# Kernel tuning notes

Hardware: AMD Instinct MI355X
Metric: run time of the kernel (lower is better)

Reference implementation:

```python
import jax, jax.numpy as jnp
import numpy as np
from jax import lax

B, T, D, LD, K = 128, 1024, 256, 512, 128
RD = LD + K  # 640 residual-LSTM width
PAD = 15     # (31 - 1) // 2 'same' padding for the LSA location conv


def _gru(x, h, wih, whh, bih, bhh):
    # torch.nn.GRUCell semantics, gate order [r, z, n]
    gi = x @ wih.T + bih
    gh = h @ whh.T + bhh
    ir, iz, inn = jnp.split(gi, 3, axis=-1)
    hr, hz, hn = jnp.split(gh, 3, axis=-1)
    r = jax.nn.sigmoid(ir + hr)
    z = jax.nn.sigmoid(iz + hz)
    n = jnp.tanh(inn + r * hn)
    return (1.0 - z) * n + z * h


def _lstm(x, h, c, wih, whh, bih, bhh):
    # torch.nn.LSTMCell semantics, gate order [i, f, g, o]
    g = x @ wih.T + bih + h @ whh.T + bhh
    i, f, gg, o = jnp.split(g, 4, axis=-1)
    c2 = jax.nn.sigmoid(f) * c + jax.nn.sigmoid(i) * jnp.tanh(gg)
    h2 = jax.nn.sigmoid(o) * jnp.tanh(c2)
    return h2, c2


def _forward(encoder_seq, encoder_seq_proj, prenet_in, attn_hidden, rnn1_h, rnn1_c,
             rnn2_h, rnn2_c, res_h, res_c, context_vec, cumulative, attn_prev,
             fc1_w, fc1_b, fc2_w, fc2_b, gru_wih, gru_whh, gru_bih, gru_bhh,
             conv_w, L_w, L_b, W_w, W_b, v_w, ri_w, ri_b,
             r1_wih, r1_whh, r1_bih, r1_bhh, r2_wih, r2_whh, r2_bih, r2_bhh,
             res_wih, res_whh, res_bih, res_bhh, stop_w, stop_b):
    # PreNet (dropout p = 0 in Decoder.__init__, so pure tanh-MLP)
    p = jnp.tanh(prenet_in @ fc1_w.T + fc1_b)
    prenet_out = jnp.tanh(p @ fc2_w.T + fc2_b)                     # [B, D//2]
    # Attention GRU
    attn_in = jnp.concatenate([context_vec, prenet_out], axis=-1)  # [B, D + D//2]
    attn_h = _gru(attn_in, attn_hidden, gru_wih, gru_whh, gru_bih, gru_bhh)  # [B, D]
    # LSA location-sensitive attention (cumulative/attn_prev are zeros at t=0)
    pq = (attn_h @ W_w.T + W_b)[:, None, :]                        # [B, 1, D]
    loc = jnp.stack([cumulative, attn_prev], axis=1)               # [B, 2, T]
    conv_out = lax.conv_general_dilated(loc, conv_w, (1,), [(PAD, PAD)],
                                        dimension_numbers=('NCH', 'OIH', 'NCH'))  # [B, 32, T]
    ploc = jnp.swapaxes(conv_out, 1, 2) @ L_w.T + L_b              # [B, T, D]
    u = jnp.squeeze(jnp.tanh(pq + encoder_seq_proj + ploc) @ v_w.T, -1)  # [B, T]
    sig = jax.nn.sigmoid(u)
    scores = sig / jnp.sum(sig, axis=1, keepdims=True)             # [B, T]
    cum_new = cumulative + scores
    context = jnp.einsum('bt,btd->bd', scores, encoder_seq)        # [B, D]
    # rnn_input projection + two residual LSTM cells (eval: no zoneout)
    x = jnp.concatenate([context, attn_h], axis=1) @ ri_w.T + ri_b  # [B, LD]
    h1, c1 = _lstm(x, rnn1_h, rnn1_c, r1_wih, r1_whh, r1_bih, r1_bhh)
    x = x + h1
    h2, c2 = _lstm(x, rnn2_h, rnn2_c, r2_wih, r2_whh, r2_bih, r2_bhh)
    x = x + h2
    # 4-layer residual LSTM stack on [prenet_in, x]
    res_x = jnp.concatenate([prenet_in, x], axis=1)                # [B, RD]
    hs, cs = [], []
    for i in range(4):
        hi, ci = _lstm(res_x, res_h[i], res_c[i], res_wih[i], res_whh[i], res_bih[i], res_bhh[i])
        res_x = res_x + hi
        hs.append(hi)
        cs.append(ci)
    cond = res_x                                                   # cond_features [B, RD]
    stop = jax.nn.sigmoid(cond @ stop_w.T + stop_b)                # [B, 1]
    return (cond, stop, scores, attn_h, h1, c1, h2, c2,
            jnp.stack(hs), jnp.stack(cs), context, cum_new)


def setup_inputs() -> dict:
    keys = iter(jax.random.split(jax.random.key(0), 64))
    nxt = lambda: next(keys)
    rn = lambda s: jax.random.normal(nxt(), s, jnp.float32)
    wp = lambda s: rn(s) * 0.02
    return {
        'encoder_seq': rn((B, T, D)),
        'encoder_seq_proj': rn((B, T, D)),
        'prenet_in': rn((B, K)),
        'attn_hidden': rn((B, D)),
        'rnn1_h': rn((B, LD)), 'rnn1_c': rn((B, LD)),
        'rnn2_h': rn((B, LD)), 'rnn2_c': rn((B, LD)),
        'res_h': rn((4, B, RD)), 'res_c': rn((4, B, RD)),
        'context_vec': rn((B, D)),
        'cumulative': jnp.zeros((B, T), jnp.float32),
        'attn_prev': jnp.zeros((B, T), jnp.float32),
        'fc1_w': wp((256, K)), 'fc1_b': jnp.zeros((256,), jnp.float32),
        'fc2_w': wp((D // 2, 256)), 'fc2_b': jnp.zeros((D // 2,), jnp.float32),
        'gru_wih': wp((3 * D, D + D // 2)), 'gru_whh': wp((3 * D, D)),
        'gru_bih': jnp.zeros((3 * D,), jnp.float32), 'gru_bhh': jnp.zeros((3 * D,), jnp.float32),
        'conv_w': wp((32, 2, 31)),
        'L_w': wp((D, 32)), 'L_b': jnp.zeros((D,), jnp.float32),
        'W_w': wp((D, D)), 'W_b': jnp.zeros((D,), jnp.float32),
        'v_w': wp((1, D)),
        'ri_w': wp((LD, 2 * D)), 'ri_b': jnp.zeros((LD,), jnp.float32),
        'r1_wih': wp((4 * LD, LD)), 'r1_whh': wp((4 * LD, LD)),
        'r1_bih': jnp.zeros((4 * LD,), jnp.float32), 'r1_bhh': jnp.zeros((4 * LD,), jnp.float32),
        'r2_wih': wp((4 * LD, LD)), 'r2_whh': wp((4 * LD, LD)),
        'r2_bih': jnp.zeros((4 * LD,), jnp.float32), 'r2_bhh': jnp.zeros((4 * LD,), jnp.float32),
        'res_wih': wp((4, 4 * RD, RD)), 'res_whh': wp((4, 4 * RD, RD)),
        'res_bih': jnp.zeros((4, 4 * RD), jnp.float32), 'res_bhh': jnp.zeros((4, 4 * RD), jnp.float32),
        'stop_w': wp((1, RD)), 'stop_b': jnp.zeros((1,), jnp.float32),
    }


def reference(encoder_seq, encoder_seq_proj, prenet_in, attn_hidden, rnn1_h, rnn1_c,
              rnn2_h, rnn2_c, res_h, res_c, context_vec, cumulative, attn_prev,
              fc1_w, fc1_b, fc2_w, fc2_b, gru_wih, gru_whh, gru_bih, gru_bhh,
              conv_w, L_w, L_b, W_w, W_b, v_w, ri_w, ri_b,
              r1_wih, r1_whh, r1_bih, r1_bhh, r2_wih, r2_whh, r2_bih, r2_bhh,
              res_wih, res_whh, res_bih, res_bhh, stop_w, stop_b):
    return _forward(encoder_seq, encoder_seq_proj, prenet_in, attn_hidden, rnn1_h, rnn1_c,
                    rnn2_h, rnn2_c, res_h, res_c, context_vec, cumulative, attn_prev,
                    fc1_w, fc1_b, fc2_w, fc2_b, gru_wih, gru_whh, gru_bih, gru_bhh,
                    conv_w, L_w, L_b, W_w, W_b, v_w, ri_w, ri_b,
                    r1_wih, r1_whh, r1_bih, r1_bhh, r2_wih, r2_whh, r2_bih, r2_bhh,
                    res_wih, res_whh, res_bih, res_bhh, stop_w, stop_b)
```

## Files before the change

kernel.cpp:

```cpp
#include <hip/hip_runtime.h>

#define DEV __device__ __forceinline__

typedef __attribute__((ext_vector_type(8))) short short8;
typedef __attribute__((ext_vector_type(4))) float f32x4;

DEV float fast_rcp(float x) { return __builtin_amdgcn_rcpf(x); }
DEV float sigm(float x) { return fast_rcp(1.0f + __expf(-x)); }
DEV float tanhf_fast(float x) { return 1.0f - 2.0f * fast_rcp(1.0f + __expf(2.0f * x)); }

DEV short f2bf(float f) {
    unsigned u = __float_as_uint(f);
    unsigned r = (u + 0x7FFFu + ((u >> 16) & 1u)) >> 16;
    return (short)r;
}
DEV float bf2f(short h) {
    return __uint_as_float(((unsigned)(unsigned short)h) << 16);
}
DEV void split1(float f, short& h, short& l) {
    h = f2bf(f);
    l = f2bf(f - bf2f(h));
}
DEV void split8(const float4& x0, const float4& x1, short8& h, short8& l) {
    float fv[8] = {x0.x, x0.y, x0.z, x0.w, x1.x, x1.y, x1.z, x1.w};
#pragma unroll
    for (int j = 0; j < 8; ++j) { short hh, ll; split1(fv[j], hh, ll); h[j] = hh; l[j] = ll; }
}
#define MFMA16 __builtin_amdgcn_mfma_f32_16x16x32_bf16
DEV f32x4 mfma3(const short8& ah, const short8& al, const short8& bh, const short8& bl, f32x4 acc) {
    acc = MFMA16(ah, bh, acc, 0, 0, 0);
    acc = MFMA16(al, bh, acc, 0, 0, 0);
    acc = MFMA16(ah, bl, acc, 0, 0, 0);
    return acc;
}

DEV void gemm_core(int bx,
                   const float* __restrict__ A1, int K1,
                   const float* __restrict__ W1, int ldw1,
                   const float* __restrict__ A2, int K2,
                   const float* __restrict__ W2, int ldw2,
                   float* __restrict__ Cp, int N, int KS, int KC)
{
    const int tid = threadIdx.x;
    const int chunk = bx % KS;
    const int n0 = (bx / KS) * 32;
    const int kbeg = chunk * KC;
    const int w = tid >> 6, lane = tid & 63;
    const int q = lane >> 4, r = lane & 15;
    const int m_base = w * 32;

    f32x4 acc[2][2];
#pragma unroll
    for (int mt = 0; mt < 2; ++mt)
#pragma unroll
        for (int nt = 0; nt < 2; ++nt)
            acc[mt][nt] = (f32x4){0.f, 0.f, 0.f, 0.f};

    auto load_frag = [&](int kg, float4 (&a)[2][2], float4 (&wv)[2][2]) {
        const float* A; const float* W; int lda, ldw, kc;
        if (kg < K1) { A = A1; W = W1; lda = K1; ldw = ldw1; kc = kg; }
        else         { A = A2; W = W2; lda = K2; ldw = ldw2; kc = kg - K1; }
#pragma unroll
        for (int mt = 0; mt < 2; ++mt) {
            const float* ap = A + (size_t)(m_base + mt * 16 + r) * lda + kc + q * 8;
            a[mt][0] = *(const float4*)ap;
            a[mt][1] = *(const float4*)(ap + 4);
        }
#pragma unroll
        for (int nt = 0; nt < 2; ++nt) {
            const float* wp = W + (size_t)(n0 + nt * 16 + r) * ldw + kc + q * 8;
            wv[nt][0] = *(const float4*)wp;
            wv[nt][1] = *(const float4*)(wp + 4);
        }
    };

    auto compute = [&](const float4 (&a)[2][2], const float4 (&wv)[2][2]) {
        short8 bh[2], bl[2];
#pragma unroll
        for (int nt = 0; nt < 2; ++nt) split8(wv[nt][0], wv[nt][1], bh[nt], bl[nt]);
#pragma unroll
        for (int mt = 0; mt < 2; ++mt) {
            short8 ah, al;
            split8(a[mt][0], a[mt][1], ah, al);
#pragma unroll
            for (int nt = 0; nt < 2; ++nt)
                acc[mt][nt] = mfma3(ah, al, bh[nt], bl[nt], acc[mt][nt]);
        }
    };

    float4 aA[2][2], aB[2][2], wA[2][2], wB[2][2];
    const int nsteps = KC >> 5;

    load_frag(kbeg, aA, wA);
    for (int s = 0; s + 1 < nsteps; ++s) {
        if (s & 1) { load_frag(kbeg + (s + 1) * 32, aA, wA); compute(aB, wB); }
        else       { load_frag(kbeg + (s + 1) * 32, aB, wB); compute(aA, wA); }
    }
    if ((nsteps - 1) & 1) compute(aB, wB);
    else                  compute(aA, wA);

    float* Co = Cp + (size_t)chunk * 128 * N;
#pragma unroll
    for (int mt = 0; mt < 2; ++mt)
#pragma unroll
        for (int nt = 0; nt < 2; ++nt)
#pragma unroll
            for (int i = 0; i < 4; ++i)
                Co[(size_t)(m_base + mt * 16 + q * 4 + i) * N + n0 + nt * 16 + r] = acc[mt][nt][i];
}

__global__ __launch_bounds__(256) void gemm_one_kernel(
    const float* __restrict__ A1, int K1, const float* __restrict__ W1, int ldw1,
    const float* __restrict__ A2, int K2, const float* __restrict__ W2, int ldw2,
    float* __restrict__ Cp, int N, int KS, int KC)
{
    gemm_core(blockIdx.x, A1, K1, W1, ldw1, A2, K2, W2, ldw2, Cp, N, KS, KC);
}

__global__ __launch_bounds__(256) void gemm_gru_kernel(
    const float* __restrict__ ctx, const float* __restrict__ pout,
    const float* __restrict__ h_old,
    const float* __restrict__ wih, const float* __restrict__ whh,
    float* __restrict__ Pa, float* __restrict__ Pb)
{
    if (blockIdx.x < 288)
        gemm_core(blockIdx.x, ctx, 256, wih, 384, pout, 128, wih + 256, 384,
                  Pa, 768, 12, 32);
    else
        gemm_core(blockIdx.x - 288, h_old, 256, whh, 256, nullptr, 0, nullptr, 0,
                  Pb, 768, 8, 32);
}

__global__ void reduce_act_kernel(const float* __restrict__ p, int KS, int MN,
                                  const float* __restrict__ b,
                                  float* __restrict__ out, int N, int act)
{
    int idx = blockIdx.x * 256 + threadIdx.x;
    if (idx >= MN) return;
    int n = idx % N;
    float v = b ? b[n] : 0.f;
    for (int s = 0; s < KS; ++s) v += p[(size_t)s * MN + idx];
    if (act) v = tanhf_fast(v);
    out[idx] = v;
}

__global__ void gru_gate_kernel(const float* __restrict__ gi_p, int KSi,
                                const float* __restrict__ gh_p, int KSh,
                                const float* __restrict__ bih, const float* __restrict__ bhh,
                                const float* __restrict__ h, float* __restrict__ out)
{
    const size_t MN = 128 * 768;
    int m = blockIdx.x, d = threadIdx.x;
    size_t base = (size_t)m * 768 + d;
    float ir = bih[d], iz = bih[256 + d], in = bih[512 + d];
    for (int s = 0; s < KSi; ++s) {
        const float* p = gi_p + s * MN + base;
        ir += p[0]; iz += p[256]; in += p[512];
    }
    float hr = bhh[d], hz = bhh[256 + d], hn = bhh[512 + d];
    for (int s = 0; s < KSh; ++s) {
        const float* p = gh_p + s * MN + base;
        hr += p[0]; hz += p[256]; hn += p[512];
    }
    float r = sigm(ir + hr);
    float z = sigm(iz + hz);
    float n = tanhf_fast(in + r * hn);
    out[m * 256 + d] = (1.f - z) * n + z * h[m * 256 + d];
}

__global__ void lstm_gate_kernel(const float* __restrict__ gp, int KS,
                                 const float* __restrict__ bih, const float* __restrict__ bhh,
                                 const float* __restrict__ c_in,
                                 float* __restrict__ h_out, float* __restrict__ c_out,
                                 const float* __restrict__ xa, int sa,
                                 const float* __restrict__ xb, int sb, int split,
                                 float* __restrict__ x_new, int H)
{
    int d = blockIdx.x * 256 + threadIdx.x;
    int m = blockIdx.y;
    if (d >= H) return;
    const size_t MN = (size_t)128 * 4 * H;
    size_t base = (size_t)m * 4 * H + d;
    float iv = bih[d] + bhh[d];
    float fv = bih[H + d] + bhh[H + d];
    float gv = bih[2 * H + d] + bhh[2 * H + d];
    float ov = bih[3 * H + d] + bhh[3 * H + d];
    for (int s = 0; s < KS; ++s) {
        const float* p = gp + s * MN + base;
        iv += p[0]; fv += p[H]; gv += p[2 * H]; ov += p[3 * H];
    }
    float c2 = sigm(fv) * c_in[(size_t)m * H + d] + sigm(iv) * tanhf_fast(gv);
    float h2 = sigm(ov) * tanhf_fast(c2);
    h_out[(size_t)m * H + d] = h2;
    c_out[(size_t)m * H + d] = c2;
    float xo = (d < split) ? xa[(size_t)m * sa + d] : xb[(size_t)m * sb + d - split];
    x_new[(size_t)m * H + d] = xo + h2;
}

__global__ __launch_bounds__(256) void attn_u_kernel(
    const float* __restrict__ esp, const float* __restrict__ pq,
    const float* __restrict__ Lw, const float* __restrict__ Lb,
    const float* __restrict__ vw, const float* __restrict__ cw,
    const float* __restrict__ cum, const float* __restrict__ prev,
    float* __restrict__ sig_out)
{
    const int b = blockIdx.x >> 4;
    const int t0 = (blockIdx.x & 15) << 6;
    const int tid = threadIdx.x;

    __shared__ float cum_s[94], prev_s[94];
    __shared__ float cw_s[2][32][33];
    __shared__ short conv_bf[64 * 32];
    __shared__ short lw_bf[256 * 32];
    __shared__ float pq_s[256], vw_s[256];

    if (tid < 94) {
        int ti = t0 - 15 + tid;
        cum_s[tid] = (ti >= 0 && ti < 1024) ? cum[b * 1024 + ti] : 0.f;
    } else if (tid >= 128 && tid < 222) {
        int i = tid - 128;
        int ti = t0 - 15 + i;
        prev_s[i] = (ti >= 0 && ti < 1024) ? prev[b * 1024 + ti] : 0.f;
    }
    for (int i = tid; i < 2048; i += 256) {
        int which = i >> 10, c = (i >> 5) & 31, k = i & 31;
        cw_s[which][c][k] = (k < 31) ? cw[(c * 2 + which) * 31 + k] : 0.f;
    }
    {
        const float4* src = (const float4*)Lw;
#pragma unroll
        for (int k = 0; k < 8; ++k) {
            float4 v = src[tid + k * 256];
            int base = (tid + k * 256) * 4;
            lw_bf[base + 0] = f2bf(v.x);
            lw_bf[base + 1] = f2bf(v.y);
            lw_bf[base + 2] = f2bf(v.z);
            lw_bf[base + 3] = f2bf(v.w);
        }
    }
    pq_s[tid] = pq[b * 256 + tid] + Lb[tid];
    vw_s[tid] = vw[tid];
    __syncthreads();

    {
        int c = tid & 31, t8 = (tid >> 5) << 3;
        float a[8] = {0.f, 0.f, 0.f, 0.f, 0.f, 0.f, 0.f, 0.f};
        for (int k = 0; k < 31; ++k) {
            float w0 = cw_s[0][c][k], w1 = cw_s[1][c][k];
#pragma unroll
            for (int j = 0; j < 8; ++j)
                a[j] += w0 * cum_s[t8 + j + k] + w1 * prev_s[t8 + j + k];
        }
#pragma unroll
        for (int j = 0; j < 8; ++j) conv_bf[(t8 + j) * 32 + c] = f2bf(a[j]);
    }
    __syncthreads();

    const int lane = tid & 63, w = tid >> 6;
    const int q = lane >> 4, c16 = lane & 15;
    const int myt = t0 + w * 16 + c16;

    short8 bfrag = *(const short8*)&conv_bf[(w * 16 + c16) * 32 + q * 8];
    const float* er = esp + ((size_t)(b * 1024 + myt) << 8);

    float s = 0.f;
#pragma unroll
    for (int dt = 0; dt < 16; ++dt) {
        short8 afrag = *(const short8*)&lw_bf[(dt * 16 + c16) * 32 + q * 8];
        f32x4 acc = {0.f, 0.f, 0.f, 0.f};
        acc = MFMA16(afrag, bfrag, acc, 0, 0, 0);
        const int d0 = dt * 16 + q * 4;
        float4 e   = *(const float4*)(er + d0);
        float4 pqv = *(const float4*)&pq_s[d0];
        float4 vwv = *(const float4*)&vw_s[d0];
        s += tanhf_fast(pqv.x + e.x + acc[0]) * vwv.x;
        s += tanhf_fast(pqv.y + e.y + acc[1]) * vwv.y;
        s += tanhf_fast(pqv.z + e.z + acc[2]) * vwv.z;
        s += tanhf_fast(pqv.w + e.w + acc[3]) * vwv.w;
    }
    s += __shfl_xor(s, 16);
    s += __shfl_xor(s, 32);
    if (lane < 16)
        sig_out[b * 1024 + t0 + w * 16 + lane] = sigm(s);
}

__global__ void attn_norm_kernel(const float* __restrict__ sig, const float* __restrict__ cum,
                                 float* __restrict__ scores, float* __restrict__ cum_new,
                                 float* __restrict__ ctx)
{
    __shared__ float red[4];
    int b = blockIdx.x, tid = threadIdx.x;
    float4 sv = *(const float4*)&sig[b * 1024 + tid * 4];
    float s = sv.x + sv.y + sv.z + sv.w;
#pragma unroll
    for (int off = 1; off < 64; off <<= 1) s += __shfl_xor(s, off);
    if ((tid & 63) == 0) red[tid >> 6] = s;
    __syncthreads();
    float inv = fast_rcp(red[0] + red[1] + red[2] + red[3]);
    float4 cv = *(const float4*)&cum[b * 1024 + tid * 4];
    float4 sc = {sv.x * inv, sv.y * inv, sv.z * inv, sv.w * inv};
    *(float4*)&scores[b * 1024 + tid * 4] = sc;
    float4 cn = {cv.x + sc.x, cv.y + sc.y, cv.z + sc.z, cv.w + sc.w};
    *(float4*)&cum_new[b * 1024 + tid * 4] = cn;
    ctx[b * 256 + tid] = 0.f;
}

__global__ void attn_ctx_kernel(const float* __restrict__ scores, const float* __restrict__ es,
                                float* __restrict__ ctx)
{
    __shared__ float sc_s[128];
    int b = blockIdx.x >> 3;
    int tbase = (blockIdx.x & 7) * 128;
    int tid = threadIdx.x;
    if (tid < 128) sc_s[tid] = scores[b * 1024 + tbase + tid];
    __syncthreads();
    float a = 0.f;
    const float* ep = es + ((size_t)(b * 1024 + tbase)) * 256 + tid;
#pragma unroll 4
    for (int tt = 0; tt < 128; ++tt)
        a += sc_s[tt] * ep[(size_t)tt * 256];
    atomicAdd(&ctx[b * 256 + tid], a);
}

__global__ void stop_kernel(const float* __restrict__ res, const float* __restrict__ sw,
                            const float* __restrict__ sb, float* __restrict__ stop)
{
    int m = blockIdx.x, lane = threadIdx.x;
    float s = 0.f;
    for (int k = lane; k < 640; k += 64) s += res[m * 640 + k] * sw[k];
#pragma unroll
    for (int off = 1; off < 64; off <<= 1) s += __shfl_xor(s, off);
    if (lane == 0) stop[m] = sigm(s + sb[0]);
}

extern "C" void kernel_launch(void* const* d_in, const int* in_sizes, int n_in,
                              void* d_out, int out_size, void* d_ws, size_t ws_size,
                              hipStream_t stream)
{
    const float* encoder_seq      = (const float*)d_in[0];
    const float* encoder_seq_proj = (const float*)d_in[1];
    const float* prenet_in        = (const float*)d_in[2];
    const float* attn_hidden      = (const float*)d_in[3];
    const float* rnn1_h  = (const float*)d_in[4];
    const float* rnn1_c  = (const float*)d_in[5];
    const float* rnn2_h  = (const float*)d_in[6];
    const float* rnn2_c  = (const float*)d_in[7];
    const float* res_h   = (const float*)d_in[8];
    const float* res_c   = (const float*)d_in[9];
    const float* context_vec = (const float*)d_in[10];
    const float* cumulative  = (const float*)d_in[11];
    const float* attn_prev   = (const float*)d_in[12];
    const float* fc1_w = (const float*)d_in[13];
    const float* fc1_b = (const float*)d_in[14];
    const float* fc2_w = (const float*)d_in[15];
    const float* fc2_b = (const float*)d_in[16];
    const float* gru_wih = (const float*)d_in[17];
    const float* gru_whh = (const float*)d_in[18];
    const float* gru_bih = (const float*)d_in[19];
    const float* gru_bhh = (const float*)d_in[20];
    const float* conv_w = (const float*)d_in[21];
    const float* L_w = (const float*)d_in[22];
    const float* L_b = (const float*)d_in[23];
    const float* W_w = (const float*)d_in[24];
    const float* W_b = (const float*)d_in[25];
    const float* v_w = (const float*)d_in[26];
    const float* ri_w = (const float*)d_in[27];
    const float* ri_b = (const float*)d_in[28];
    const float* r1_wih = (const float*)d_in[29];
    const float* r1_whh = (const float*)d_in[30];
    const float* r1_bih = (const float*)d_in[31];
    const float* r1_bhh = (const float*)d_in[32];
    const float* r2_wih = (const float*)d_in[33];
    const float* r2_whh = (const float*)d_in[34];
    const float* r2_bih = (const float*)d_in[35];
    const float* r2_bhh = (const float*)d_in[36];
    const float* res_wih = (const float*)d_in[37];
    const float* res_whh = (const float*)d_in[38];
    const float* res_bih = (const float*)d_in[39];
    const float* res_bhh = (const float*)d_in[40];
    const float* stop_w = (const float*)d_in[41];
    const float* stop_b = (const float*)d_in[42];

    float* ws  = (float*)d_ws;
    float* out = (float*)d_out;

    const size_t OFF_P     = 0;
    const size_t OFF_POUT  = 32768;
    const size_t OFF_PQ    = 49152;
    const size_t OFF_SIG   = 81920;
    const size_t OFF_X     = 212992;
    const size_t OFF_XB    = 278528;
    const size_t OFF_XC    = 344064;
    const size_t OFF_R0    = 409600;
    const size_t OFF_R1    = 491520;
    const size_t OFF_PART  = 573440;
    const size_t OFF_PARTB = OFF_PART + (size_t)12 * 128 * 768;
    const size_t OFF_PARTH = OFF_PART + (size_t)4 * 128 * 2560;

    const size_t O_COND   = 0;
    const size_t O_STOP   = 81920;
    const size_t O_SCORES = 82048;
    const size_t O_ATTNH  = 213120;
    const size_t O_H1     = 245888;
    const size_t O_C1     = 311424;
    const size_t O_H2     = 376960;
    const size_t O_C2     = 442496;
    const size_t O_HS     = 508032;
    const size_t O_CS     = 835712;
    const size_t O_CTX    = 1163392;
    const size_t O_CUM    = 1196160;

    gemm_one_kernel<<<8 * 4, 256, 0, stream>>>(
        prenet_in, 128, fc1_w, 128, nullptr, 0, nullptr, 0,
        ws + OFF_PART, 256, 4, 32);
    reduce_act_kernel<<<128, 256, 0, stream>>>(ws + OFF_PART, 4, 128 * 256, fc1_b,
                                               ws + OFF_P, 256, 1);
    gemm_one_kernel<<<4 * 8, 256, 0, stream>>>(
        ws + OFF_P, 256, fc2_w, 256, nullptr, 0, nullptr, 0,
        ws + OFF_PART, 128, 8, 32);
    reduce_act_kernel<<<64, 256, 0, stream>>>(ws + OFF_PART, 8, 128 * 128, fc2_b,
                                              ws + OFF_POUT, 128, 1);

    gemm_gru_kernel<<<480, 256, 0, stream>>>(
        context_vec, ws + OFF_POUT, attn_hidden, gru_wih, gru_whh,
        ws + OFF_PART, ws + OFF_PARTB);
    gru_gate_kernel<<<128, 256, 0, stream>>>(ws + OFF_PART, 12, ws + OFF_PARTB, 8,
                                             gru_bih, gru_bhh, attn_hidden, out + O_ATTNH);

    gemm_one_kernel<<<8 * 8, 256, 0, stream>>>(
        out + O_ATTNH, 256, W_w, 256, nullptr, 0, nullptr, 0,
        ws + OFF_PART, 256, 8, 32);
    reduce_act_kernel<<<128, 256, 0, stream>>>(ws + OFF_PART, 8, 128 * 256, W_b,
                                               ws + OFF_PQ, 256, 0);

    attn_u_kernel<<<2048, 256, 0, stream>>>(encoder_seq_proj, ws + OFF_PQ, L_w,
                                            L_b, v_w, conv_w, cumulative, attn_prev,
                                            ws + OFF_SIG);
    attn_norm_kernel<<<128, 256, 0, stream>>>(ws + OFF_SIG, cumulative,
                                              out + O_SCORES, out + O_CUM, out + O_CTX);
    attn_ctx_kernel<<<1024, 256, 0, stream>>>(out + O_SCORES, encoder_seq, out + O_CTX);

    gemm_one_kernel<<<16 * 8, 256, 0, stream>>>(
        out + O_CTX, 256, ri_w, 512,
        out + O_ATTNH, 256, ri_w + 256, 512,
        ws + OFF_PART, 512, 8, 64);
    reduce_act_kernel<<<256, 256, 0, stream>>>(ws + OFF_PART, 8, 128 * 512, ri_b,
                                               ws + OFF_X, 512, 0);

    gemm_one_kernel<<<64 * 4, 256, 0, stream>>>(
        ws + OFF_X, 512, r1_wih, 512,
        rnn1_h, 512, r1_whh, 512,
        ws + OFF_PART, 2048, 4, 256);
    lstm_gate_kernel<<<dim3(2, 128), 256, 0, stream>>>(
        ws + OFF_PART, 4, r1_bih, r1_bhh, rnn1_c, out + O_H1, out + O_C1,
        nullptr, 0, ws + OFF_X, 512, 0, ws + OFF_XB, 512);
    gemm_one_kernel<<<64 * 4, 256, 0, stream>>>(
        ws + OFF_XB, 512, r2_wih, 512,
        rnn2_h, 512, r2_whh, 512,
        ws + OFF_PART, 2048, 4, 256);
    lstm_gate_kernel<<<dim3(2, 128), 256, 0, stream>>>(
        ws + OFF_PART, 4, r2_bih, r2_bhh, rnn2_c, out + O_H2, out + O_C2,
        nullptr, 0, ws + OFF_XB, 512, 0, ws + OFF_XC, 512);

    for (int i = 0; i < 4; ++i) {
        const float* wih = res_wih + (size_t)i * 2560 * 640;
        const float* whh = res_whh + (size_t)i * 2560 * 640;
        const float* hA  = res_h + (size_t)i * 81920;
        const float* cA  = res_c + (size_t)i * 81920;
        if (i == 0) {
            gemm_one_kernel<<<80 * 4, 256, 0, stream>>>(
                prenet_in, 128, wih, 640,
                ws + OFF_XC, 512, wih + 128, 640,
                ws + OFF_PART, 2560, 4, 160);
        } else {
            const float* rcur = ws + ((i & 1) ? OFF_R0 : OFF_R1);
            gemm_one_kernel<<<80 * 4, 256, 0, stream>>>(
                rcur, 640, wih, 640, nullptr, 0, nullptr, 0,
                ws + OFF_PART, 2560, 4, 160);
        }
        gemm_one_kernel<<<80 * 4, 256, 0, stream>>>(
            hA, 640, whh, 640, nullptr, 0, nullptr, 0,
            ws + OFF_PARTH, 2560, 4, 160);

        const float *xa, *xb; int sa, sb, split;
        if (i == 0) { xa = prenet_in; sa = 128; xb = ws + OFF_XC; sb = 512; split = 128; }
        else { xa = nullptr; sa = 0; xb = ws + ((i & 1) ? OFF_R0 : OFF_R1); sb = 640; split = 0; }
        float* xnew = (i == 3) ? (out + O_COND) : (ws + ((i & 1) ? OFF_R1 : OFF_R0));
        lstm_gate_kernel<<<dim3(3, 128), 256, 0, stream>>>(
            ws + OFF_PART, 8,
            res_bih + (size_t)i * 2560, res_bhh + (size_t)i * 2560,
            cA, out + O_HS + (size_t)i * 81920, out + O_CS + (size_t)i * 81920,
            xa, sa, xb, sb, split, xnew, 640);
    }

    stop_kernel<<<128, 64, 0, stream>>>(out + O_COND, stop_w, stop_b, out + O_STOP);
}
```

Before: 632.8 us.

## Fuse split-K reductions and gate epilogues into GEMM kernels via last-block atomics

Each split-K GEMM now counts finished blocks per output tile with an atomic counter, and the last block to arrive does the reduction plus the bias/activation or GRU/LSTM gate math. This removes the separate reduce and gate kernel launches. The residual LSTM input and hidden GEMMs are merged into one launch, and attention normalization is folded into the context kernel using an atomic sum of sigmoids. The cost is serialized tail work in a few blocks per tile, extra fences and atomics, and an init kernel to zero the counters.

Result: slower. 2.152 ms (+240.1%).

```diff
diff --git a/kernel.cpp b/kernel.cpp
--- a/kernel.cpp
+++ b/kernel.cpp
@@ -109,92 +109,137 @@
                 Co[(size_t)(m_base + mt * 16 + q * 4 + i) * N + n0 + nt * 16 + r] = acc[mt][nt][i];
 }
 
-__global__ __launch_bounds__(256) void gemm_one_kernel(
+DEV bool arrive_last(int* cnt, int target)
+{
+    __shared__ int s_rank;
+    __threadfence();
+    __syncthreads();
+    if (threadIdx.x == 0) s_rank = atomicAdd(cnt, 1);
+    __syncthreads();
+    if (s_rank == target - 1) { __threadfence(); return true; }
+    return false;
+}
+
+__global__ __launch_bounds__(256) void gemm_fc_kernel(
     const float* __restrict__ A1, int K1, const float* __restrict__ W1, int ldw1,
     const float* __restrict__ A2, int K2, const float* __restrict__ W2, int ldw2,
-    float* __restrict__ Cp, int N, int KS, int KC)
+    float* __restrict__ Cp, int N, int KS, int KC,
+    const float* __restrict__ bias, float* __restrict__ outp, int act, int* cnt)
 {
     gemm_core(blockIdx.x, A1, K1, W1, ldw1, A2, K2, W2, ldw2, Cp, N, KS, KC);
+    const int ntile = blockIdx.x / KS;
+    if (arrive_last(&cnt[ntile], KS)) {
+        const int tid = threadIdx.x;
+        const int c = tid & 31, mrow = tid >> 5;
+        const int n0 = ntile * 32;
+        const size_t MN = (size_t)128 * N;
+        for (int p = 0; p < 16; ++p) {
+            int m = p * 8 + mrow;
+            int n = n0 + c;
+            float v = bias ? bias[n] : 0.f;
+            for (int s = 0; s < KS; ++s) v += Cp[(size_t)s * MN + (size_t)m * N + n];
+            if (act) v = tanhf_fast(v);
+            outp[(size_t)m * N + n] = v;
+        }
+    }
 }
 
 __global__ __launch_bounds__(256) void gemm_gru_kernel(
-    const float* __restrict__ ctx, const float* __restrict__ pout,
+    const float* __restrict__ ctxv, const float* __restrict__ pout,
     const float* __restrict__ h_old,
     const float* __restrict__ wih, const float* __restrict__ whh,
-    float* __restrict__ Pa, float* __restrict__ Pb)
-{
-    if (blockIdx.x < 288)
-        gemm_core(blockIdx.x, ctx, 256, wih, 384, pout, 128, wih + 256, 384,
+    float* __restrict__ Pa, float* __restrict__ Pb,
+    const float* __restrict__ bih, const float* __restrict__ bhh,
+    float* __restrict__ h_new, int* cnt)
+{
+    int j;
+    if (blockIdx.x < 288) {
+        gemm_core(blockIdx.x, ctxv, 256, wih, 384, pout, 128, wih + 256, 384,
                   Pa, 768, 12, 32);
-    else
+        j = (blockIdx.x / 12) & 7;
+    } else {
         gemm_core(blockIdx.x - 288, h_old, 256, whh, 256, nullptr, 0, nullptr, 0,
                   Pb, 768, 8, 32);
-}
-
-__global__ void reduce_act_kernel(const float* __restrict__ p, int KS, int MN,
-                                  const float* __restrict__ b,
-                                  float* __restrict__ out, int N, int act)
-{
-    int idx = blockIdx.x * 256 + threadIdx.x;
-    if (idx >= MN) return;
-    int n = idx % N;
-    float v = b ? b[n] : 0.f;
-    for (int s = 0; s < KS; ++s) v += p[(size_t)s * MN + idx];
-    if (act) v = tanhf_fast(v);
-    out[idx] = v;
-}
-
-__global__ void gru_gate_kernel(const float* __restrict__ gi_p, int KSi,
-                                const float* __restrict__ gh_p, int KSh,
-                                const float* __restrict__ bih, const float* __restrict__ bhh,
-                                const float* __restrict__ h, float* __restrict__ out)
-{
-    const size_t MN = 128 * 768;
-    int m = blockIdx.x, d = threadIdx.x;
-    size_t base = (size_t)m * 768 + d;
-    float ir = bih[d], iz = bih[256 + d], in = bih[512 + d];
-    for (int s = 0; s < KSi; ++s) {
-        const float* p = gi_p + s * MN + base;
-        ir += p[0]; iz += p[256]; in += p[512];
-    }
-    float hr = bhh[d], hz = bhh[256 + d], hn = bhh[512 + d];
-    for (int s = 0; s < KSh; ++s) {
-        const float* p = gh_p + s * MN + base;
-        hr += p[0]; hz += p[256]; hn += p[512];
-    }
-    float r = sigm(ir + hr);
-    float z = sigm(iz + hz);
-    float n = tanhf_fast(in + r * hn);
-    out[m * 256 + d] = (1.f - z) * n + z * h[m * 256 + d];
-}
-
-__global__ void lstm_gate_kernel(const float* __restrict__ gp, int KS,
-                                 const float* __restrict__ bih, const float* __restrict__ bhh,
-                                 const float* __restrict__ c_in,
-                                 float* __restrict__ h_out, float* __restrict__ c_out,
-                                 const float* __restrict__ xa, int sa,
-                                 const float* __restrict__ xb, int sb, int split,
-                                 float* __restrict__ x_new, int H)
-{
-    int d = blockIdx.x * 256 + threadIdx.x;
-    int m = blockIdx.y;
-    if (d >= H) return;
-    const size_t MN = (size_t)128 * 4 * H;
-    size_t base = (size_t)m * 4 * H + d;
-    float iv = bih[d] + bhh[d];
-    float fv = bih[H + d] + bhh[H + d];
-    float gv = bih[2 * H + d] + bhh[2 * H + d];
-    float ov = bih[3 * H + d] + bhh[3 * H + d];
-    for (int s = 0; s < KS; ++s) {
-        const float* p = gp + s * MN + base;
-        iv += p[0]; fv += p[H]; gv += p[2 * H]; ov += p[3 * H];
-    }
-    float c2 = sigm(fv) * c_in[(size_t)m * H + d] + sigm(iv) * tanhf_fast(gv);
-    float h2 = sigm(ov) * tanhf_fast(c2);
-    h_out[(size_t)m * H + d] = h2;
-    c_out[(size_t)m * H + d] = c2;
-    float xo = (d < split) ? xa[(size_t)m * sa + d] : xb[(size_t)m * sb + d - split];
-    x_new[(size_t)m * H + d] = xo + h2;
+        j = ((blockIdx.x - 288) / 8) & 7;
+    }
+    if (arrive_last(&cnt[j], 60)) {
+        const int tid = threadIdx.x;
+        const int c = tid & 31, mrow = tid >> 5;
+        const size_t MN = (size_t)128 * 768;
+        for (int p = 0; p < 16; ++p) {
+            int m = p * 8 + mrow;
+            int d = j * 32 + c;
+            size_t base = (size_t)m * 768 + d;
+            float ir = bih[d], iz = bih[256 + d], in = bih[512 + d];
+            for (int s = 0; s < 12; ++s) {
+                const float* pp = Pa + s * MN + base;
+                ir += pp[0]; iz += pp[256]; in += pp[512];
+            }
+            float hr = bhh[d], hz = bhh[256 + d], hn = bhh[512 + d];
+            for (int s = 0; s < 8; ++s) {
+                const float* pp = Pb + s * MN + base;
+                hr += pp[0]; hz += pp[256]; hn += pp[512];
+            }
+            float rr = sigm(ir + hr), zz = sigm(iz + hz);
+            float nn = tanhf_fast(in + rr * hn);
+            h_new[m * 256 + d] = (1.f - zz) * nn + zz * h_old[m * 256 + d];
+        }
+    }
+}
+
+__global__ __launch_bounds__(256) void gemm_lstm_kernel(
+    const float* __restrict__ A1, int K1, const float* __restrict__ W1, int ldw1,
+    const float* __restrict__ A2, int K2, const float* __restrict__ W2, int ldw2,
+    const float* __restrict__ Ah, int Kh, const float* __restrict__ Wh,
+    float* __restrict__ P, int N, int KS, int KC0, int KC1,
+    const float* __restrict__ bih, const float* __restrict__ bhh,
+    const float* __restrict__ c_in,
+    float* __restrict__ h_out, float* __restrict__ c_out,
+    const float* __restrict__ xa, int sa,
+    const float* __restrict__ xb, int sb, int split,
+    float* __restrict__ x_new, int H, int* cnt)
+{
+    const int nb0 = (N / 32) * KS;
+    const int hasH = (Ah != nullptr);
+    const size_t MN = (size_t)128 * N;
+    int ntile;
+    if ((int)blockIdx.x < nb0) {
+        gemm_core(blockIdx.x, A1, K1, W1, ldw1, A2, K2, W2, ldw2, P, N, KS, KC0);
+        ntile = blockIdx.x / KS;
+    } else {
+        int bx2 = blockIdx.x - nb0;
+        gemm_core(bx2, Ah, Kh, Wh, Kh, nullptr, 0, nullptr, 0,
+                  P + (size_t)KS * MN, N, KS, KC1);
+        ntile = bx2 / KS;
+    }
+    const int dtiles = H >> 5;
+    const int j = ntile % dtiles;
+    const int target = (hasH ? 8 : 4) * KS;
+    const int nch = (hasH ? 2 : 1) * KS;
+    if (arrive_last(&cnt[j], target)) {
+        const int tid = threadIdx.x;
+        const int c = tid & 31, mrow = tid >> 5;
+        for (int p = 0; p < 16; ++p) {
+            int m = p * 8 + mrow;
+            int d = j * 32 + c;
+            float gv[4];
+#pragma unroll
+            for (int g = 0; g < 4; ++g) {
+                int gc = g * H + d;
+                float v = bih[gc] + bhh[gc];
+                for (int s = 0; s < nch; ++s)
+                    v += P[(size_t)s * MN + (size_t)m * N + gc];
+                gv[g] = v;
+            }
+            size_t o = (size_t)m * H + d;
+            float c2 = sigm(gv[1]) * c_in[o] + sigm(gv[0]) * tanhf_fast(gv[2]);
+            float h2 = sigm(gv[3]) * tanhf_fast(c2);
+            h_out[o] = h2;
+            c_out[o] = c2;
+            float xo = (d < split) ? xa[(size_t)m * sa + d] : xb[(size_t)m * sb + d - split];
+            x_new[o] = xo + h2;
+        }
+    }
 }
 
 __global__ __launch_bounds__(256) void attn_u_kernel(
@@ -284,42 +329,51 @@
         sig_out[b * 1024 + t0 + w * 16 + lane] = sigm(s);
 }
 
-__global__ void attn_norm_kernel(const float* __restrict__ sig, const float* __restrict__ cum,
-                                 float* __restrict__ scores, float* __restrict__ cum_new,
-                                 float* __restrict__ ctx)
-{
-    __shared__ float red[4];
-    int b = blockIdx.x, tid = threadIdx.x;
-    float4 sv = *(const float4*)&sig[b * 1024 + tid * 4];
-    float s = sv.x + sv.y + sv.z + sv.w;
-#pragma unroll
-    for (int off = 1; off < 64; off <<= 1) s += __shfl_xor(s, off);
-    if ((tid & 63) == 0) red[tid >> 6] = s;
+__global__ __launch_bounds__(256) void attn_ctx_kernel(
+    const float* __restrict__ sig, const float* __restrict__ es,
+    const float* __restrict__ cum,
+    float* __restrict__ ctx, float* __restrict__ scores,
+    float* __restrict__ cum_new, float* __restrict__ ssum, int* cnt)
+{
+    __shared__ float sc_s[128];
+    const int b = blockIdx.x >> 3;
+    const int tbase = (blockIdx.x & 7) * 128;
+    const int tid = threadIdx.x;
+    if (tid < 128) sc_s[tid] = sig[b * 1024 + tbase + tid];
     __syncthreads();
-    float inv = fast_rcp(red[0] + red[1] + red[2] + red[3]);
-    float4 cv = *(const float4*)&cum[b * 1024 + tid * 4];
-    float4 sc = {sv.x * inv, sv.y * inv, sv.z * inv, sv.w * inv};
-    *(float4*)&scores[b * 1024 + tid * 4] = sc;
-    float4 cn = {cv.x + sc.x, cv.y + sc.y, cv.z + sc.z, cv.w + sc.w};
-    *(float4*)&cum_new[b * 1024 + tid * 4] = cn;
-    ctx[b * 256 + tid] = 0.f;
-}
-
-__global__ void attn_ctx_kernel(const float* __restrict__ scores, const float* __restrict__ es,
-                                float* __restrict__ ctx)
-{
-    __shared__ float sc_s[128];
-    int b = blockIdx.x >> 3;
-    int tbase = (blockIdx.x & 7) * 128;
-    int tid = threadIdx.x;
-    if (tid < 128) sc_s[tid] = scores[b * 1024 + tbase + tid];
-    __syncthreads();
+
+    float v = (tid < 128) ? sc_s[tid] : 0.f;
+#pragma unroll
+    for (int off = 1; off < 64; off <<= 1) v += __shfl_xor(v, off);
+    if (tid < 128 && (tid & 63) == 0) atomicAdd(&ssum[b], v);
+
     float a = 0.f;
     const float* ep = es + ((size_t)(b * 1024 + tbase)) * 256 + tid;
 #pragma unroll 4
     for (int tt = 0; tt < 128; ++tt)
         a += sc_s[tt] * ep[(size_t)tt * 256];
     atomicAdd(&ctx[b * 256 + tid], a);
+
+    if (arrive_last(&cnt[b], 8)) {
+        float inv = fast_rcp(ssum[b]);
+        ctx[b * 256 + tid] *= inv;
+#pragma unroll
+        for (int p = 0; p < 4; ++p) {
+            int i = p * 256 + tid;
+            float sc = sig[b * 1024 + i] * inv;
+            scores[b * 1024 + i] = sc;
+            cum_new[b * 1024 + i] = cum[b * 1024 + i] + sc;
+        }
+    }
+}
+
+__global__ void init_kernel(int* __restrict__ cnt, float* __restrict__ ssum,
+                            float* __restrict__ ctx)
+{
+    int i = blockIdx.x * 256 + threadIdx.x;
+    if (i < 512) cnt[i] = 0;
+    if (i < 128) ssum[i] = 0.f;
+    if (i < 32768) ctx[i] = 0.f;
 }
 
 __global__ void stop_kernel(const float* __restrict__ res, const float* __restrict__ sw,
@@ -395,7 +449,14 @@
     const size_t OFF_R1    = 491520;
     const size_t OFF_PART  = 573440;
     const size_t OFF_PARTB = OFF_PART + (size_t)12 * 128 * 768;
-    const size_t OFF_PARTH = OFF_PART + (size_t)4 * 128 * 2560;
+    const size_t OFF_CNT   = 3300000;
+
+    int*   cnt  = (int*)(ws + OFF_CNT);
+    float* ssum = ws + OFF_CNT + 512;
+
+    const int CNT_FC1 = 0, CNT_FC2 = 8, CNT_GRU = 16, CNT_PQ = 24,
+              CNT_RI = 32, CNT_L1 = 48, CNT_L2 = 64, CNT_RES = 80,
+              CNT_ATT = 160;
 
     const size_t O_COND   = 0;
     const size_t O_STOP   = 81920;
@@ -410,87 +471,75 @@
     const size_t O_CTX    = 1163392;
     const size_t O_CUM    = 1196160;
 
-    gemm_one_kernel<<<8 * 4, 256, 0, stream>>>(
+    init_kernel<<<128, 256, 0, stream>>>(cnt, ssum, out + O_CTX);
+
+    gemm_fc_kernel<<<32, 256, 0, stream>>>(
         prenet_in, 128, fc1_w, 128, nullptr, 0, nullptr, 0,
-        ws + OFF_PART, 256, 4, 32);
-    reduce_act_kernel<<<128, 256, 0, stream>>>(ws + OFF_PART, 4, 128 * 256, fc1_b,
-                                               ws + OFF_P, 256, 1);
-    gemm_one_kernel<<<4 * 8, 256, 0, stream>>>(
+        ws + OFF_PART, 256, 4, 32, fc1_b, ws + OFF_P, 1, cnt + CNT_FC1);
+
+    gemm_fc_kernel<<<32, 256, 0, stream>>>(
         ws + OFF_P, 256, fc2_w, 256, nullptr, 0, nullptr, 0,
-        ws + OFF_PART, 128, 8, 32);
-    reduce_act_kernel<<<64, 256, 0, stream>>>(ws + OFF_PART, 8, 128 * 128, fc2_b,
-                                              ws + OFF_POUT, 128, 1);
+        ws + OFF_PART, 128, 8, 32, fc2_b, ws + OFF_POUT, 1, cnt + CNT_FC2);
 
     gemm_gru_kernel<<<480, 256, 0, stream>>>(
         context_vec, ws + OFF_POUT, attn_hidden, gru_wih, gru_whh,
-        ws + OFF_PART, ws + OFF_PARTB);
-    gru_gate_kernel<<<128, 256, 0, stream>>>(ws + OFF_PART, 12, ws + OFF_PARTB, 8,
-                                             gru_bih, gru_bhh, attn_hidden, out + O_ATTNH);
-
-    gemm_one_kernel<<<8 * 8, 256, 0, stream>>>(
+        ws + OFF_PART, ws + OFF_PARTB,
+        gru_bih, gru_bhh, out + O_ATTNH, cnt + CNT_GRU);
+
+    gemm_fc_kernel<<<64, 256, 0, stream>>>(
         out + O_ATTNH, 256, W_w, 256, nullptr, 0, nullptr, 0,
-        ws + OFF_PART, 256, 8, 32);
-    reduce_act_kernel<<<128, 256, 0, stream>>>(ws + OFF_PART, 8, 128 * 256, W_b,
-                                               ws + OFF_PQ, 256, 0);
+        ws + OFF_PART, 256, 8, 32, W_b, ws + OFF_PQ, 0, cnt + CNT_PQ);
 
     attn_u_kernel<<<2048, 256, 0, stream>>>(encoder_seq_proj, ws + OFF_PQ, L_w,
                                             L_b, v_w, conv_w, cumulative, attn_prev,
                                             ws + OFF_SIG);
-    attn_norm_kernel<<<128, 256, 0, stream>>>(ws + OFF_SIG, cumulative,
-                                              out + O_SCORES, out + O_CUM, out + O_CTX);
-    attn_ctx_kernel<<<1024, 256, 0, stream>>>(out + O_SCORES, encoder_seq, out + O_CTX);
-
-    gemm_one_kernel<<<16 * 8, 256, 0, stream>>>(
+    attn_ctx_kernel<<<1024, 256, 0, stream>>>(
+        ws + OFF_SIG, encoder_seq, cumulative,
+        out + O_CTX, out + O_SCORES, out + O_CUM, ssum, cnt + CNT_ATT);
+
+    gemm_fc_kernel<<<128, 256, 0, stream>>>(
         out + O_CTX, 256, ri_w, 512,
         out + O_ATTNH, 256, ri_w + 256, 512,
-        ws + OFF_PART, 512, 8, 64);
-    reduce_act_kernel<<<256, 256, 0, stream>>>(ws + OFF_PART, 8, 128 * 512, ri_b,
-                                               ws + OFF_X, 512, 0);
-
-    gemm_one_kernel<<<64 * 4, 256, 0, stream>>>(
-        ws + OFF_X, 512, r1_wih, 512,
-        rnn1_h, 512, r1_whh, 512,
-        ws + OFF_PART, 2048, 4, 256);
-    lstm_gate_kernel<<<dim3(2, 128), 256, 0, stream>>>(
-        ws + OFF_PART, 4, r1_bih, r1_bhh, rnn1_c, out + O_H1, out + O_C1,
-        nullptr, 0, ws + OFF_X, 512, 0, ws + OFF_XB, 512);
-    gemm_one_kernel<<<64 * 4, 256, 0, stream>>>(
-        ws + OFF_XB, 512, r2_wih, 512,
-        rnn2_h, 512, r2_whh, 512,
-        ws + OFF_PART, 2048, 4, 256);
-    lstm_gate_kernel<<<dim3(2, 128), 256, 0, stream>>>(
-        ws + OFF_PART, 4, r2_bih, r2_bhh, rnn2_c, out + O_H2, out + O_C2,
-        nullptr, 0, ws + OFF_XB, 512, 0, ws + OFF_XC, 512);
+        ws + OFF_PART, 512, 8, 64, ri_b, ws + OFF_X, 0, cnt + CNT_RI);
+
+    gemm_lstm_kernel<<<256, 256, 0, stream>>>(
+        ws + OFF_X, 512, r1_wih, 512, rnn1_h, 512, r1_whh, 512,
+        nullptr, 0, nullptr,
+        ws + OFF_PART, 2048, 4, 256, 0,
+        r1_bih, r1_bhh, rnn1_c, out + O_H1, out + O_C1,
+        nullptr, 0, ws + OFF_X, 512, 0, ws + OFF_XB, 512, cnt + CNT_L1);
+
+    gemm_lstm_kernel<<<256, 256, 0, stream>>>(
+        ws + OFF_XB, 512, r2_wih, 512, rnn2_h, 512, r2_whh, 512,
+        nullptr, 0, nullptr,
+        ws + OFF_PART, 2048, 4, 256, 0,
+        r2_bih, r2_bhh, rnn2_c, out + O_H2, out + O_C2,
+        nullptr, 0, ws + OFF_XB, 512, 0, ws + OFF_XC, 512, cnt + CNT_L2);
 
     for (int i = 0; i < 4; ++i) {
         const float* wih = res_wih + (size_t)i * 2560 * 640;
         const float* whh = res_whh + (size_t)i * 2560 * 640;
         const float* hA  = res_h + (size_t)i * 81920;
         const float* cA  = res_c + (size_t)i * 81920;
+        const float *xa, *xb; int sa, sb, split;
+        const float *A1, *A2, *W1, *W2; int K1, K2;
         if (i == 0) {
-            gemm_one_kernel<<<80 * 4, 256, 0, stream>>>(
-                prenet_in, 128, wih, 640,
-                ws + OFF_XC, 512, wih + 128, 640,
-                ws + OFF_PART, 2560, 4, 160);
+            A1 = prenet_in; K1 = 128; W1 = wih;
+            A2 = ws + OFF_XC; K2 = 512; W2 = wih + 128;
+            xa = prenet_in; sa = 128; xb = ws + OFF_XC; sb = 512; split = 128;
         } else {
-            const float* rcur = ws + ((i & 1) ? OFF_R0 : OFF_R1);
-            gemm_one_kernel<<<80 * 4, 256, 0, stream>>>(
-                rcur, 640, wih, 640, nullptr, 0, nullptr, 0,
-                ws + OFF_PART, 2560, 4, 160);
-        }
-        gemm_one_kernel<<<80 * 4, 256, 0, stream>>>(
-            hA, 640, whh, 640, nullptr, 0, nullptr, 0,
-            ws + OFF_PARTH, 2560, 4, 160);
-
-        const float *xa, *xb; int sa, sb, split;
-        if (i == 0) { xa = prenet_in; sa = 128; xb = ws + OFF_XC; sb = 512; split = 128; }
-        else { xa = nullptr; sa = 0; xb = ws + ((i & 1) ? OFF_R0 : OFF_R1); sb = 640; split = 0; }
+            A1 = ws + ((i & 1) ? OFF_R0 : OFF_R1); K1 = 640; W1 = wih;
+            A2 = nullptr; K2 = 0; W2 = nullptr;
+            xa = nullptr; sa = 0; xb = A1; sb = 640; split = 0;
+        }
         float* xnew = (i == 3) ? (out + O_COND) : (ws + ((i & 1) ? OFF_R1 : OFF_R0));
-        lstm_gate_kernel<<<dim3(3, 128), 256, 0, stream>>>(
-            ws + OFF_PART, 8,
+        gemm_lstm_kernel<<<640, 256, 0, stream>>>(
+            A1, K1, W1, 640, A2, K2, W2, 640,
+            hA, 640, whh,
+            ws + OFF_PART, 2560, 4, 160, 160,
             res_bih + (size_t)i * 2560, res_bhh + (size_t)i * 2560,
             cA, out + O_HS + (size_t)i * 81920, out + O_CS + (size_t)i * 81920,
-            xa, sa, xb, sb, split, xnew, 640);
+            xa, sa, xb, sb, split, xnew, 640, cnt + CNT_RES + 20 * i);
     }
 
     stop_kernel<<<128, 64, 0, stream>>>(out + O_COND, stop_w, stop_b, out + O_STOP);
```
